# Performance work log

Hardware: AMD Instinct MI355X
Metric: run time of the kernel (lower is better)

Reference implementation:

```python
import jax, jax.numpy as jnp
import numpy as np

MARGIN = 0.5
EPS = 1e-6  # torch F.pairwise_distance adds eps to the difference before the norm
B, N, D = 1024, 1024, 64


def setup_inputs() -> dict:
    key = jax.random.key(0)
    ka, kp, kn = jax.random.split(key, 3)
    anchor = jax.random.normal(ka, (B, N, D), dtype=jnp.float32)
    positive = jax.random.normal(kp, (B, N, D), dtype=jnp.float32)
    negative = jax.random.normal(kn, (B, N, D), dtype=jnp.float32)
    return {"anchor": anchor, "positive": positive, "negative": negative}


def reference(anchor, positive, negative):
    # pairwise L2 distances over the feature dim -> [B, N]
    dist_pos = jnp.linalg.norm(anchor - positive + EPS, axis=-1)
    dist_neg = jnp.linalg.norm(anchor - negative + EPS, axis=-1)

    # hard-negative mining, vectorized over the batch:
    # candidates are columns where dist_pos - dist_neg + margin > 0;
    # among candidates pick the column with the LARGEST dist_neg
    diff = dist_pos - dist_neg + MARGIN            # [B, N]
    valid = diff > 0                               # [B, N]
    neg_scores = jnp.where(valid, dist_neg, -jnp.inf)
    sel_col = jnp.argmax(neg_scores, axis=1)       # [B] column index of hard negative

    # faithful to the original: negative is indexed on its FIRST dim with the
    # selected column index (requires B == N), yielding [B, N, D]
    hard_neg = negative[sel_col]
    has_valid = jnp.any(valid, axis=1)             # rows the original would keep

    loss = jnp.mean(jax.nn.relu(MARGIN + dist_pos - dist_neg))
    return loss, hard_neg, has_valid
```

## Files before the change

### kernel.cpp

```cpp
#include <hip/hip_runtime.h>
#include <math.h>

#define BB 1024
#define NN 1024
#define DD 64
#define MARGIN_V 0.5f
#define EPS_V 1e-6f

__global__ __launch_bounds__(256) void k_dist(const float* __restrict__ a,
                                              const float* __restrict__ p,
                                              const float* __restrict__ g,
                                              float* __restrict__ ws_loss,
                                              int* __restrict__ ws_sel,
                                              float* __restrict__ out_hasvalid)
{
    const int b    = blockIdx.x;
    const int tid  = threadIdx.x;
    const int lane = tid & 63;
    const int wave = tid >> 6;
    const int grp  = lane >> 4;
    const int gl   = lane & 15;

    const size_t base = (size_t)b * NN * DD;

    float loss_acc   = 0.f;
    float best_score = -INFINITY;
    int   best_idx   = 0;
    int   any_valid  = 0;

    for (int i = 0; i < NN / 16; ++i) {
        const int n = i * 16 + wave * 4 + grp;
        const size_t off = base + (size_t)n * DD + (size_t)gl * 4;
        const float4 va = *(const float4*)(a + off);
        const float4 vp = *(const float4*)(p + off);
        const float4 vg = *(const float4*)(g + off);

        float dp = 0.f, dn = 0.f, t;
        t = va.x - vp.x + EPS_V; dp += t * t;
        t = va.y - vp.y + EPS_V; dp += t * t;
        t = va.z - vp.z + EPS_V; dp += t * t;
        t = va.w - vp.w + EPS_V; dp += t * t;
        t = va.x - vg.x + EPS_V; dn += t * t;
        t = va.y - vg.y + EPS_V; dn += t * t;
        t = va.z - vg.z + EPS_V; dn += t * t;
        t = va.w - vg.w + EPS_V; dn += t * t;

        for (int m = 1; m < 16; m <<= 1) {
            dp += __shfl_xor(dp, m, 64);
            dn += __shfl_xor(dn, m, 64);
        }

        if (gl == 0) {
            const float dist_pos = sqrtf(dp);
            const float dist_neg = sqrtf(dn);
            const float diff = MARGIN_V + dist_pos - dist_neg;
            loss_acc += fmaxf(diff, 0.f);
            const bool valid = diff > 0.f;
            any_valid |= (int)valid;
            const float score = valid ? dist_neg : -INFINITY;
            if (score > best_score) { best_score = score; best_idx = n; }
        }
    }

    __shared__ float s_score[16];
    __shared__ int   s_idx[16];
    __shared__ float s_loss[16];
    __shared__ int   s_valid[16];
    if (gl == 0) {
        const int slot = wave * 4 + grp;
        s_score[slot] = best_score;
        s_idx[slot]   = best_idx;
        s_loss[slot]  = loss_acc;
        s_valid[slot] = any_valid;
    }
    __syncthreads();
    if (tid == 0) {
        float bs = s_score[0]; int bi = s_idx[0];
        float ls = s_loss[0];  int av = s_valid[0];
        for (int k = 1; k < 16; ++k) {
            const float sc = s_score[k]; const int ix = s_idx[k];
            if (sc > bs || (sc == bs && ix < bi)) { bs = sc; bi = ix; }
            ls += s_loss[k];
            av |= s_valid[k];
        }
        ws_loss[b] = ls;
        ws_sel[b]  = bi;
        out_hasvalid[b] = av ? 1.0f : 0.0f;
    }
}

__global__ __launch_bounds__(1024) void k_loss(const float* __restrict__ ws_loss,
                                               float* __restrict__ out_loss)
{
    __shared__ float s[16];
    const int t = threadIdx.x;
    float v = ws_loss[t];
    for (int m = 1; m < 64; m <<= 1) v += __shfl_xor(v, m, 64);
    if ((t & 63) == 0) s[t >> 6] = v;
    __syncthreads();
    if (t == 0) {
        float tot = 0.f;
        for (int k = 0; k < 16; ++k) tot += s[k];
        out_loss[0] = tot / (float)((size_t)BB * NN);
    }
}

__global__ __launch_bounds__(256) void k_gather(const float* __restrict__ g,
                                                const int* __restrict__ ws_sel,
                                                float* __restrict__ out_hn)
{
    const int b   = blockIdx.y;
    const int sel = ws_sel[b];
    const float* __restrict__ src = g      + (size_t)sel * (NN * DD);
    float* __restrict__       dst = out_hn + (size_t)b   * (NN * DD);
    const int t = blockIdx.x * blockDim.x + threadIdx.x;
    #pragma unroll
    for (int k = 0; k < (NN * DD) / 8192; ++k) {
        const int idx = t + k * 8192;
        dst[idx] = src[idx];
    }
}

extern "C" void kernel_launch(void* const* d_in, const int* in_sizes, int n_in,
                              void* d_out, int out_size, void* d_ws, size_t ws_size,
                              hipStream_t stream) {
    const float* anchor   = (const float*)d_in[0];
    const float* positive = (const float*)d_in[1];
    const float* negative = (const float*)d_in[2];
    float* out = (float*)d_out;

    float* out_loss     = out;
    float* out_hard_neg = out + 1;
    float* out_hasvalid = out + 1 + (size_t)BB * NN * DD;

    float* ws_loss = (float*)d_ws;
    int*   ws_sel  = (int*)((float*)d_ws + BB);

    k_dist<<<dim3(BB), dim3(256), 0, stream>>>(anchor, positive, negative,
                                               ws_loss, ws_sel, out_hasvalid);
    k_loss<<<dim3(1), dim3(1024), 0, stream>>>(ws_loss, out_loss);
    k_gather<<<dim3(32, BB), dim3(256), 0, stream>>>(negative, ws_sel, out_hard_neg);
}
```

Measured before the change: 261.8 us.

## Split distance kernel across four column quarters per row with merge kernel

The distance pass now launches four blocks per batch row, each covering a quarter of the columns. It also processes two columns per loop iteration so more loads are in flight at once. A new merge kernel combines the per-quarter best score, index, validity and loss partials, and writes the selection and has_valid outputs. The goal is more blocks to fill the GPU and better latency hiding on a memory-bound pass, at the cost of a slightly more complex reduction and extra workspace traffic.

```diff
diff --git a/kernel.cpp b/kernel.cpp
--- a/kernel.cpp
+++ b/kernel.cpp
@@ -6,59 +6,94 @@
 #define DD 64
 #define MARGIN_V 0.5f
 #define EPS_V 1e-6f
+#define QSPLIT 4
+#define QCOLS (NN / QSPLIT)
 
 __global__ __launch_bounds__(256) void k_dist(const float* __restrict__ a,
                                               const float* __restrict__ p,
                                               const float* __restrict__ g,
                                               float* __restrict__ ws_loss,
-                                              int* __restrict__ ws_sel,
-                                              float* __restrict__ out_hasvalid)
+                                              float* __restrict__ ws_score,
+                                              int* __restrict__ ws_idx,
+                                              int* __restrict__ ws_valid)
 {
-    const int b    = blockIdx.x;
+    const int blk  = blockIdx.x;
+    const int b    = blk >> 2;
+    const int q    = blk & 3;
     const int tid  = threadIdx.x;
     const int lane = tid & 63;
     const int wave = tid >> 6;
     const int grp  = lane >> 4;
     const int gl   = lane & 15;
-
-    const size_t base = (size_t)b * NN * DD;
+    const int group = wave * 4 + grp;
+
+    const size_t base  = (size_t)b * (NN * DD);
+    const int    ncol0 = q * QCOLS + group;
 
     float loss_acc   = 0.f;
     float best_score = -INFINITY;
     int   best_idx   = 0;
     int   any_valid  = 0;
 
-    for (int i = 0; i < NN / 16; ++i) {
-        const int n = i * 16 + wave * 4 + grp;
-        const size_t off = base + (size_t)n * DD + (size_t)gl * 4;
-        const float4 va = *(const float4*)(a + off);
-        const float4 vp = *(const float4*)(p + off);
-        const float4 vg = *(const float4*)(g + off);
-
-        float dp = 0.f, dn = 0.f, t;
-        t = va.x - vp.x + EPS_V; dp += t * t;
-        t = va.y - vp.y + EPS_V; dp += t * t;
-        t = va.z - vp.z + EPS_V; dp += t * t;
-        t = va.w - vp.w + EPS_V; dp += t * t;
-        t = va.x - vg.x + EPS_V; dn += t * t;
-        t = va.y - vg.y + EPS_V; dn += t * t;
-        t = va.z - vg.z + EPS_V; dn += t * t;
-        t = va.w - vg.w + EPS_V; dn += t * t;
+    for (int j = 0; j < 8; ++j) {
+        const int n0 = ncol0 + j * 32;
+        const int n1 = n0 + 16;
+        const size_t off0 = base + (size_t)n0 * DD + (size_t)gl * 4;
+        const size_t off1 = off0 + (size_t)16 * DD;
+
+        const float4 va0 = *(const float4*)(a + off0);
+        const float4 vp0 = *(const float4*)(p + off0);
+        const float4 vg0 = *(const float4*)(g + off0);
+        const float4 va1 = *(const float4*)(a + off1);
+        const float4 vp1 = *(const float4*)(p + off1);
+        const float4 vg1 = *(const float4*)(g + off1);
+
+        float dp0 = 0.f, dn0 = 0.f, dp1 = 0.f, dn1 = 0.f, t;
+        t = va0.x - vp0.x + EPS_V; dp0 += t * t;
+        t = va0.y - vp0.y + EPS_V; dp0 += t * t;
+        t = va0.z - vp0.z + EPS_V; dp0 += t * t;
+        t = va0.w - vp0.w + EPS_V; dp0 += t * t;
+        t = va0.x - vg0.x + EPS_V; dn0 += t * t;
+        t = va0.y - vg0.y + EPS_V; dn0 += t * t;
+        t = va0.z - vg0.z + EPS_V; dn0 += t * t;
+        t = va0.w - vg0.w + EPS_V; dn0 += t * t;
+        t = va1.x - vp1.x + EPS_V; dp1 += t * t;
+        t = va1.y - vp1.y + EPS_V; dp1 += t * t;
+        t = va1.z - vp1.z + EPS_V; dp1 += t * t;
+        t = va1.w - vp1.w + EPS_V; dp1 += t * t;
+        t = va1.x - vg1.x + EPS_V; dn1 += t * t;
+        t = va1.y - vg1.y + EPS_V; dn1 += t * t;
+        t = va1.z - vg1.z + EPS_V; dn1 += t * t;
+        t = va1.w - vg1.w + EPS_V; dn1 += t * t;
 
         for (int m = 1; m < 16; m <<= 1) {
-            dp += __shfl_xor(dp, m, 64);
-            dn += __shfl_xor(dn, m, 64);
+            dp0 += __shfl_xor(dp0, m, 64);
+            dn0 += __shfl_xor(dn0, m, 64);
+            dp1 += __shfl_xor(dp1, m, 64);
+            dn1 += __shfl_xor(dn1, m, 64);
         }
 
         if (gl == 0) {
-            const float dist_pos = sqrtf(dp);
-            const float dist_neg = sqrtf(dn);
-            const float diff = MARGIN_V + dist_pos - dist_neg;
-            loss_acc += fmaxf(diff, 0.f);
-            const bool valid = diff > 0.f;
-            any_valid |= (int)valid;
-            const float score = valid ? dist_neg : -INFINITY;
-            if (score > best_score) { best_score = score; best_idx = n; }
+            {
+                const float dist_pos = sqrtf(dp0);
+                const float dist_neg = sqrtf(dn0);
+                const float diff = MARGIN_V + dist_pos - dist_neg;
+                loss_acc += fmaxf(diff, 0.f);
+                const bool valid = diff > 0.f;
+                any_valid |= (int)valid;
+                const float score = valid ? dist_neg : -INFINITY;
+                if (score > best_score) { best_score = score; best_idx = n0; }
+            }
+            {
+                const float dist_pos = sqrtf(dp1);
+                const float dist_neg = sqrtf(dn1);
+                const float diff = MARGIN_V + dist_pos - dist_neg;
+                loss_acc += fmaxf(diff, 0.f);
+                const bool valid = diff > 0.f;
+                any_valid |= (int)valid;
+                const float score = valid ? dist_neg : -INFINITY;
+                if (score > best_score) { best_score = score; best_idx = n1; }
+            }
         }
     }
 
@@ -67,11 +102,10 @@
     __shared__ float s_loss[16];
     __shared__ int   s_valid[16];
     if (gl == 0) {
-        const int slot = wave * 4 + grp;
-        s_score[slot] = best_score;
-        s_idx[slot]   = best_idx;
-        s_loss[slot]  = loss_acc;
-        s_valid[slot] = any_valid;
+        s_score[group] = best_score;
+        s_idx[group]   = best_idx;
+        s_loss[group]  = loss_acc;
+        s_valid[group] = any_valid;
     }
     __syncthreads();
     if (tid == 0) {
@@ -83,22 +117,43 @@
             ls += s_loss[k];
             av |= s_valid[k];
         }
-        ws_loss[b] = ls;
-        ws_sel[b]  = bi;
-        out_hasvalid[b] = av ? 1.0f : 0.0f;
-    }
-}
-
-__global__ __launch_bounds__(1024) void k_loss(const float* __restrict__ ws_loss,
-                                               float* __restrict__ out_loss)
+        ws_loss[blk]  = ls;
+        ws_score[blk] = bs;
+        ws_idx[blk]   = bi;
+        ws_valid[blk] = av;
+    }
+}
+
+__global__ __launch_bounds__(1024) void k_merge(const float* __restrict__ ws_loss,
+                                                const float* __restrict__ ws_score,
+                                                const int* __restrict__ ws_idx,
+                                                const int* __restrict__ ws_valid,
+                                                float* __restrict__ out_loss,
+                                                int* __restrict__ ws_sel,
+                                                float* __restrict__ out_hasvalid)
 {
+    const int b = threadIdx.x;
+    float ls = 0.f;
+    float bs = -INFINITY;
+    int   bi = 0x7fffffff;
+    int   av = 0;
+    for (int qq = 0; qq < QSPLIT; ++qq) {
+        const int idx = b * QSPLIT + qq;
+        const float sc = ws_score[idx];
+        const int   ix = ws_idx[idx];
+        if (sc > bs || (sc == bs && ix < bi)) { bs = sc; bi = ix; }
+        ls += ws_loss[idx];
+        av |= ws_valid[idx];
+    }
+    ws_sel[b] = bi;
+    out_hasvalid[b] = av ? 1.0f : 0.0f;
+
     __shared__ float s[16];
-    const int t = threadIdx.x;
-    float v = ws_loss[t];
+    float v = ls;
     for (int m = 1; m < 64; m <<= 1) v += __shfl_xor(v, m, 64);
-    if ((t & 63) == 0) s[t >> 6] = v;
+    if ((b & 63) == 0) s[b >> 6] = v;
     __syncthreads();
-    if (t == 0) {
+    if (b == 0) {
         float tot = 0.f;
         for (int k = 0; k < 16; ++k) tot += s[k];
         out_loss[0] = tot / (float)((size_t)BB * NN);
@@ -133,11 +188,15 @@
     float* out_hard_neg = out + 1;
     float* out_hasvalid = out + 1 + (size_t)BB * NN * DD;
 
-    float* ws_loss = (float*)d_ws;
-    int*   ws_sel  = (int*)((float*)d_ws + BB);
-
-    k_dist<<<dim3(BB), dim3(256), 0, stream>>>(anchor, positive, negative,
-                                               ws_loss, ws_sel, out_hasvalid);
-    k_loss<<<dim3(1), dim3(1024), 0, stream>>>(ws_loss, out_loss);
+    float* ws_loss  = (float*)d_ws;
+    float* ws_score = ws_loss + BB * QSPLIT;
+    int*   ws_idx   = (int*)(ws_score + BB * QSPLIT);
+    int*   ws_valid = ws_idx + BB * QSPLIT;
+    int*   ws_sel   = ws_valid + BB * QSPLIT;
+
+    k_dist<<<dim3(BB * QSPLIT), dim3(256), 0, stream>>>(anchor, positive, negative,
+                                                        ws_loss, ws_score, ws_idx, ws_valid);
+    k_merge<<<dim3(1), dim3(1024), 0, stream>>>(ws_loss, ws_score, ws_idx, ws_valid,
+                                                out_loss, ws_sel, out_hasvalid);
     k_gather<<<dim3(32, BB), dim3(256), 0, stream>>>(negative, ws_sel, out_hard_neg);
 }
```

After: 266.0 us. Within noise of the previous version (+1.6%).
